# Kernel optimization log

Measured on AMD Instinct MI355X. Metric: run time of the kernel, lower is better.

The kernel has to match this reference:

```python
import jax, jax.numpy as jnp
import numpy as np

B, S, D, H = 4, 2048, 512, 8
DH = D // H


def setup_inputs() -> dict:
    key = jax.random.key(0)
    ks = jax.random.split(key, 6)
    embeddings = jax.random.normal(ks[0], (B, S, D), dtype=jnp.float32)
    token_masks = jax.random.randint(ks[1], (B, S), 0, 2, dtype=jnp.int32)
    # keras 'random_normal' initializer: stddev 0.05
    Wq = 0.05 * jax.random.normal(ks[2], (D, D), dtype=jnp.float32)
    Wk = 0.05 * jax.random.normal(ks[3], (D, D), dtype=jnp.float32)
    Wv = 0.05 * jax.random.normal(ks[4], (D, D), dtype=jnp.float32)
    Wo = 0.05 * jax.random.normal(ks[5], (D, D), dtype=jnp.float32)
    return {"embeddings": embeddings, "token_masks": token_masks,
            "Wq": Wq, "Wk": Wk, "Wv": Wv, "Wo": Wo}


def reference(embeddings, token_masks, Wq, Wk, Wv, Wo):
    b, s, d = embeddings.shape
    h, dh = H, d // H
    # QKV projections -> (b, h, s, dh)
    def split_heads(x):
        return x.reshape(b, s, h, dh).transpose(0, 2, 1, 3)
    Q = split_heads(embeddings @ Wq)
    K = split_heads(embeddings @ Wk)
    V = split_heads(embeddings @ Wv)
    scores = jnp.einsum('bhqd,bhkd->bhqk', Q, K) / jnp.sqrt(jnp.float32(dh))
    # causal (lower-triangular) mask combined with padding mask on both q and k
    causal = jnp.tril(jnp.ones((s, s), dtype=jnp.float32))
    tm = token_masks.astype(jnp.float32)
    attn_mask = causal[None, None, :, :] * tm[:, None, None, :] * tm[:, None, :, None]
    scores = jnp.where(attn_mask > 0, scores, jnp.float32(-1e30))
    weights = jax.nn.softmax(scores, axis=-1)  # dropout omitted (inference/eval mode)
    context = jnp.einsum('bhqk,bhkd->bhqd', weights, V)
    context = context.transpose(0, 2, 1, 3).reshape(b, s, d)
    return context @ Wo
```

## Files before the change

kernel.cpp:

```cpp
#include <hip/hip_runtime.h>
#include <hip/hip_bf16.h>
#include <stdint.h>

#define BATCH 4
#define SEQ 2048
#define DMODEL 512
#define NHEAD 8
#define HD 64

#define C1 0.18033688f
#define BIAS2 -23.0831207f

using f32x4 = __attribute__((ext_vector_type(4))) float;
using bfrag = __attribute__((ext_vector_type(8))) short;

__device__ __forceinline__ short f2bf(float f) {
  uint32_t x = __builtin_bit_cast(uint32_t, f);
  uint32_t r = (x + 0x7fffu + ((x >> 16) & 1u)) >> 16;
  return (short)r;
}
__device__ __forceinline__ short f2bf_fast(float f) {
  return (short)((__builtin_bit_cast(uint32_t, f) + 0x8000u) >> 16);
}
__device__ __forceinline__ float bf2f(short s) {
  return __builtin_bit_cast(float, ((uint32_t)(uint16_t)s) << 16);
}
__device__ __forceinline__ void gl_lds16(const void* g, void* l) {
  __builtin_amdgcn_global_load_lds(
      (const __attribute__((address_space(1))) void*)g,
      (__attribute__((address_space(3))) void*)l, 16, 0, 0);
}
__device__ __forceinline__ bool sniff_f32(const void* p, int tid) {
  const uint32_t* xw = (const uint32_t*)p;
  const int lane = tid & 63;
  const uint32_t w1 = xw[lane], w2 = xw[64 + lane];
  bool bad = (((w1 >> 7) & 0xffu) >= 0xB0u) | (((w1 >> 23) & 0xffu) >= 0xB0u) |
             (((w2 >> 7) & 0xffu) >= 0xB0u) | (((w2 >> 23) & 0xffu) >= 0xB0u);
  return __ballot(bad) != 0ull;
}

__global__ __launch_bounds__(256) void prep(const void* __restrict__ X,
                                            const void* __restrict__ w0,
                                            const void* __restrict__ w1,
                                            const void* __restrict__ w2,
                                            const void* __restrict__ w3,
                                            short* __restrict__ Xb,
                                            short* __restrict__ wtAll,
                                            float* __restrict__ mv) {
  const int blk = blockIdx.x, tid = threadIdx.x;
  if (blk < 2048) {
    const bool isf32 = sniff_f32(X, tid);
    const int i = (blk * 256 + tid) * 8;
    if (isf32) {
      const float* f = (const float*)X;
      short r[8];
#pragma unroll
      for (int j = 0; j < 8; ++j) r[j] = f2bf(f[i + j]);
      *(bfrag*)&Xb[i] = *(bfrag*)r;
    } else {
      *(bfrag*)&Xb[i] = *(const bfrag*)&((const short*)X)[i];
    }
  } else if (blk < 3072) {
    __shared__ short t[32][33];
    const int idx = blk - 2048;
    const int z = idx >> 8, rem = idx & 255;
    const void* in = (z == 0) ? w0 : (z == 1) ? w1 : (z == 2) ? w2 : w3;
    short* out = wtAll + (size_t)z * DMODEL * DMODEL;
    const int tx = tid & 31, ty = tid >> 5;
    const bool isf32 = sniff_f32(in, tid);
    const int n0 = (rem & 15) * 32, k0 = (rem >> 4) * 32;
#pragma unroll
    for (int i = ty; i < 32; i += 8) {
      const int idx2 = (k0 + i) * DMODEL + n0 + tx;
      t[i][tx] = isf32 ? f2bf(((const float*)in)[idx2]) : ((const short*)in)[idx2];
    }
    __syncthreads();
#pragma unroll
    for (int i = ty; i < 32; i += 8) out[(n0 + i) * DMODEL + k0 + tx] = t[tx][i];
  } else {
#pragma unroll
    for (int j = 0; j < 8; ++j) mv[tid * 8 + j] = 0.f;
  }
}

__global__ __launch_bounds__(256) void gemm_qkv(const short* __restrict__ X,
                                                const short* __restrict__ WtAll,
                                                short* __restrict__ Qo,
                                                short* __restrict__ Ko,
                                                short* __restrict__ Vo,
                                                float* __restrict__ mv) {
  __shared__ __align__(16) short As[128 * 32];
  __shared__ __align__(16) short Bs[128 * 32];
  const int which = blockIdx.z;
  const short* Wt = WtAll + which * DMODEL * DMODEL;
  const int m0 = blockIdx.y * 128, n0 = blockIdx.x * 128;
  const int tid = threadIdx.x, lane = tid & 63, wave = tid >> 6;
  const int l15 = lane & 15, quad = lane >> 4;
  const int wm = wave >> 1, wn = wave & 1;
  const int lrow = lane >> 2, lcol = (lane & 3) * 8;
  f32x4 acc[4][4] = {};
  for (int kc = 0; kc < DMODEL; kc += 32) {
#pragma unroll
    for (int i = 0; i < 2; ++i) {
      const int r0 = (wave * 2 + i) * 16;
      gl_lds16(&X[(size_t)(m0 + r0 + lrow) * DMODEL + kc + lcol], &As[r0 * 32]);
      gl_lds16(&Wt[(size_t)(n0 + r0 + lrow) * DMODEL + kc + lcol], &Bs[r0 * 32]);
    }
    __syncthreads();
    bfrag a[4], b[4];
#pragma unroll
    for (int t = 0; t < 4; ++t) {
      a[t] = *(const bfrag*)&As[(wm * 64 + t * 16 + l15) * 32 + quad * 8];
      b[t] = *(const bfrag*)&Bs[(wn * 64 + t * 16 + l15) * 32 + quad * 8];
    }
#pragma unroll
    for (int tm = 0; tm < 4; ++tm)
#pragma unroll
      for (int tn = 0; tn < 4; ++tn)
        acc[tm][tn] = __builtin_amdgcn_mfma_f32_16x16x32_bf16(a[tm], b[tn], acc[tm][tn], 0, 0, 0);
    __syncthreads();
  }
  short* O = (which == 0) ? Qo : (which == 1) ? Ko : Vo;
#pragma unroll
  for (int tn = 0; tn < 4; ++tn) {
    const int col = n0 + wn * 64 + tn * 16 + l15;
    const int h = col >> 6, d = col & 63;
#pragma unroll
    for (int tm = 0; tm < 4; ++tm) {
#pragma unroll
      for (int r = 0; r < 4; ++r) {
        const int row = m0 + wm * 64 + tm * 16 + quad * 4 + r;
        const int b = row >> 11, s = row & 2047;
        O[((b * NHEAD + h) * SEQ + s) * HD + d] = f2bf(acc[tm][tn][r]);
      }
    }
  }
  if (which == 2) {
    const int b = (m0 + wm * 64) >> 11;
#pragma unroll
    for (int tn = 0; tn < 4; ++tn) {
      float s = 0.f;
#pragma unroll
      for (int tm = 0; tm < 4; ++tm)
#pragma unroll
        for (int r = 0; r < 4; ++r) s += acc[tm][tn][r];
      s += __shfl_xor(s, 16);
      s += __shfl_xor(s, 32);
      if (quad == 0) {
        const int col = n0 + wn * 64 + tn * 16 + l15;
        const int h = col >> 6, d = col & 63;
        atomicAdd(&mv[(b * NHEAD + h) * 64 + d], s);
      }
    }
  }
}

__global__ __launch_bounds__(256) void gemm_out(const short* __restrict__ X,
                                                const short* __restrict__ Wt,
                                                float* __restrict__ O) {
  __shared__ __align__(16) short As[128 * 32];
  __shared__ __align__(16) short Bs[128 * 32];
  const int m0 = blockIdx.y * 128, n0 = blockIdx.x * 128;
  const int tid = threadIdx.x, lane = tid & 63, wave = tid >> 6;
  const int l15 = lane & 15, quad = lane >> 4;
  const int wm = wave >> 1, wn = wave & 1;
  const int lrow = lane >> 2, lcol = (lane & 3) * 8;
  f32x4 acc[4][4] = {};
  for (int kc = 0; kc < DMODEL; kc += 32) {
#pragma unroll
    for (int i = 0; i < 2; ++i) {
      const int r0 = (wave * 2 + i) * 16;
      gl_lds16(&X[(size_t)(m0 + r0 + lrow) * DMODEL + kc + lcol], &As[r0 * 32]);
      gl_lds16(&Wt[(size_t)(n0 + r0 + lrow) * DMODEL + kc + lcol], &Bs[r0 * 32]);
    }
    __syncthreads();
    bfrag a[4], b[4];
#pragma unroll
    for (int t = 0; t < 4; ++t) {
      a[t] = *(const bfrag*)&As[(wm * 64 + t * 16 + l15) * 32 + quad * 8];
      b[t] = *(const bfrag*)&Bs[(wn * 64 + t * 16 + l15) * 32 + quad * 8];
    }
#pragma unroll
    for (int tm = 0; tm < 4; ++tm)
#pragma unroll
      for (int tn = 0; tn < 4; ++tn)
        acc[tm][tn] = __builtin_amdgcn_mfma_f32_16x16x32_bf16(a[tm], b[tn], acc[tm][tn], 0, 0, 0);
    __syncthreads();
  }
#pragma unroll
  for (int tm = 0; tm < 4; ++tm)
#pragma unroll
    for (int tn = 0; tn < 4; ++tn) {
      const int col = n0 + wn * 64 + tn * 16 + l15;
#pragma unroll
      for (int r = 0; r < 4; ++r) {
        const int row = m0 + wm * 64 + tm * 16 + quad * 4 + r;
        O[(size_t)row * DMODEL + col] = acc[tm][tn][r];
      }
    }
}

__global__ __launch_bounds__(256, 4) void attn(const short* __restrict__ Q,
                                               const short* __restrict__ K,
                                               const short* __restrict__ V,
                                               const int* __restrict__ tmask,
                                               const float* __restrict__ meanV,
                                               short* __restrict__ ctx) {
  __shared__ __align__(16) short Ks[64 * 72];
  __shared__ __align__(16) short Vts[64 * 64];
  __shared__ __align__(16) short Ps[4 * 16 * 64];
  __shared__ int tmq[64];
  __shared__ int tmk[64];
  const int m2 = blockIdx.x >> 3, a3 = blockIdx.x & 7;
  const int j2 = blockIdx.y >> 3, b3 = blockIdx.y & 7;
  const int quart = (m2 + j2) & 3;
  const int qi = quart * 8 + ((quart & 1) ? (7 - a3) : a3);
  const int bh = j2 * 8 + b3;
  const int b = bh >> 3, h = bh & 7;
  const int q0 = qi * 64;
  const int tid = threadIdx.x, lane = tid & 63, wave = tid >> 6;
  const int l15 = lane & 15, quad = lane >> 4;
  const size_t base = (size_t)bh * SEQ * HD;

  bfrag qa0 = *(const bfrag*)&Q[base + (size_t)(q0 + wave * 16 + l15) * HD + quad * 8];
  bfrag qa1 = *(const bfrag*)&Q[base + (size_t)(q0 + wave * 16 + l15) * HD + 32 + quad * 8];
  if (tid < 64) tmq[tid] = tmask[b * SEQ + q0 + tid];

  f32x4 accO[4] = {};
  float lrow[4] = {0.f, 0.f, 0.f, 0.f};

  const int rp = tid >> 3, sgp = tid & 7;
  bfrag kA, kB, vA, vB;
  int tmreg = 0;

  auto prefetch = [&](int kc) {
    const size_t o0 = base + (size_t)(kc + 2 * rp) * HD + sgp * 8;
    kA = *(const bfrag*)&K[o0];
    kB = *(const bfrag*)&K[o0 + HD];
    vA = *(const bfrag*)&V[o0];
    vB = *(const bfrag*)&V[o0 + HD];
    if (tid < 64) tmreg = tmask[b * SEQ + kc + tid];
  };
  auto store_lds = [&]() {
    *(bfrag*)&Ks[(2 * rp) * 72 + sgp * 8] = kA;
    *(bfrag*)&Ks[(2 * rp + 1) * 72 + sgp * 8] = kB;
    const int g = ((rp >> 2) ^ ((sgp & 1) << 2) ^ (sgp >> 1)) & 7;
    const int kpos = (2 * rp) & 7;
#pragma unroll
    for (int j = 0; j < 8; ++j) {
      const uint32_t w = (uint32_t)(uint16_t)vA[j] | ((uint32_t)(uint16_t)vB[j] << 16);
      *(uint32_t*)&Vts[(sgp * 8 + j) * 64 + g * 8 + kpos] = w;
    }
    if (tid < 64) tmk[tid] = tmreg;
  };
  auto compute = [&](bool diag) {
    f32x4 sacc[4] = {};
#pragma unroll
    for (int t = 0; t < 4; ++t) {
      bfrag b0 = *(const bfrag*)&Ks[(t * 16 + l15) * 72 + quad * 8];
      sacc[t] = __builtin_amdgcn_mfma_f32_16x16x32_bf16(qa0, b0, sacc[t], 0, 0, 0);
    }
#pragma unroll
    for (int t = 0; t < 4; ++t) {
      bfrag b1 = *(const bfrag*)&Ks[(t * 16 + l15) * 72 + 32 + quad * 8];
      sacc[t] = __builtin_amdgcn_mfma_f32_16x16x32_bf16(qa1, b1, sacc[t], 0, 0, 0);
    }
    float badd[4];
#pragma unroll
    for (int t = 0; t < 4; ++t) badd[t] = tmk[t * 16 + l15] ? BIAS2 : -1e30f;
#pragma unroll
    for (int r = 0; r < 4; ++r) {
      const int m = quad * 4 + r;
#pragma unroll
      for (int t = 0; t < 4; ++t) {
        float p = exp2f(fmaf(sacc[t][r], C1, badd[t]));
        if (diag && (t * 16 + l15 > wave * 16 + m)) p = 0.f;
        lrow[r] += p;
        const int g = ((t * 2 + (l15 >> 3)) ^ (m & 7) ^ ((m >> 3) << 1)) & 7;
        Ps[wave * 1024 + m * 64 + g * 8 + (l15 & 7)] = f2bf_fast(p);
      }
    }
#pragma unroll
    for (int ks = 0; ks < 2; ++ks) {
#pragma unroll
      for (int t = 0; t < 4; ++t) {
        const int gp = ((ks * 4 + quad) ^ (l15 & 7) ^ ((l15 >> 3) << 1)) & 7;
        bfrag pa = *(const bfrag*)&Ps[wave * 1024 + l15 * 64 + gp * 8];
        const int d = t * 16 + l15;
        const int gv = ((ks * 4 + quad) ^ ((l15 >> 3) << 2) ^ t) & 7;
        bfrag vb = *(const bfrag*)&Vts[d * 64 + gv * 8];
        accO[t] = __builtin_amdgcn_mfma_f32_16x16x32_bf16(pa, vb, accO[t], 0, 0, 0);
      }
    }
  };

  prefetch(0);
  for (int kc = 0; kc <= q0; kc += 64) {
    __syncthreads();
    store_lds();
    __syncthreads();
    if (kc < q0) prefetch(kc + 64);
    compute(kc == q0);
  }

#pragma unroll
  for (int r = 0; r < 4; ++r) {
    float l = lrow[r];
    l += __shfl_xor(l, 1);
    l += __shfl_xor(l, 2);
    l += __shfl_xor(l, 4);
    l += __shfl_xor(l, 8);
    lrow[r] = 1.f / l;
  }
  const int qrow_loc = wave * 16 + quad * 4;
#pragma unroll
  for (int t = 0; t < 4; ++t) {
    const int d = t * 16 + l15;
    const float mvd = meanV[bh * 64 + d] * (1.f / 2048.f);
#pragma unroll
    for (int r = 0; r < 4; ++r) {
      const int row = qrow_loc + r;
      float val = accO[t][r] * lrow[r];
      if (tmq[row] == 0) val = mvd;
      ctx[((size_t)(b * SEQ + q0 + row)) * DMODEL + h * HD + d] = f2bf(val);
    }
  }
}

extern "C" void kernel_launch(void* const* d_in, const int* in_sizes, int n_in,
                              void* d_out, int out_size, void* d_ws, size_t ws_size,
                              hipStream_t stream) {
  const void* X = d_in[0];
  const int* tmask = (const int*)d_in[1];
  const void* Wq = d_in[2];
  const void* Wk = d_in[3];
  const void* Wv = d_in[4];
  const void* Wo = d_in[5];
  float* out = (float*)d_out;
  char* ws = (char*)d_ws;

  const size_t WELEM = (size_t)DMODEL * DMODEL;
  const size_t TELEM = (size_t)BATCH * NHEAD * SEQ * HD;

  float* mv = (float*)(ws + 4096);
  short* wt = (short*)(ws + 4096 + 8192);
  short* Xb = (short*)(ws + 4096 + 8192 + 2097152);
  short* Qb = Xb + TELEM;
  short* Kb = Qb + TELEM;
  short* Vb = Kb + TELEM;
  short* Cb = Vb + TELEM;

  prep<<<3073, 256, 0, stream>>>(X, Wq, Wk, Wv, Wo, Xb, wt, mv);
  gemm_qkv<<<dim3(4, 64, 3), 256, 0, stream>>>(Xb, wt, Qb, Kb, Vb, mv);
  attn<<<dim3(32, 32), 256, 0, stream>>>(Qb, Kb, Vb, tmask, mv, Cb);
  gemm_out<<<dim3(4, 64), 256, 0, stream>>>(Cb, wt + 3 * WELEM, out);
}
```

Baseline: 172.8 us.

## Split key tile across waves in attention, keep probabilities in registers

```diff
diff --git a/kernel.cpp b/kernel.cpp
--- a/kernel.cpp
+++ b/kernel.cpp
@@ -13,6 +13,8 @@
 
 using f32x4 = __attribute__((ext_vector_type(4))) float;
 using bfrag = __attribute__((ext_vector_type(8))) short;
+using u32x4 = __attribute__((ext_vector_type(4))) unsigned int;
+using s4 = __attribute__((ext_vector_type(4))) short;
 
 __device__ __forceinline__ short f2bf(float f) {
   uint32_t x = __builtin_bit_cast(uint32_t, f);
@@ -29,6 +31,11 @@
   __builtin_amdgcn_global_load_lds(
       (const __attribute__((address_space(1))) void*)g,
       (__attribute__((address_space(3))) void*)l, 16, 0, 0);
+}
+__device__ __forceinline__ uint32_t cvtpk(float lo, float hi) {
+  uint32_t r;
+  asm("v_cvt_pk_bf16_f32 %0, %1, %2" : "=v"(r) : "v"(lo), "v"(hi));
+  return r;
 }
 __device__ __forceinline__ bool sniff_f32(const void* p, int tid) {
   const uint32_t* xw = (const uint32_t*)p;
@@ -200,17 +207,15 @@
     }
 }
 
-__global__ __launch_bounds__(256, 4) void attn(const short* __restrict__ Q,
+__global__ __launch_bounds__(256, 3) void attn(const short* __restrict__ Q,
                                                const short* __restrict__ K,
                                                const short* __restrict__ V,
                                                const int* __restrict__ tmask,
                                                const float* __restrict__ meanV,
                                                short* __restrict__ ctx) {
-  __shared__ __align__(16) short Ks[64 * 72];
-  __shared__ __align__(16) short Vts[64 * 64];
-  __shared__ __align__(16) short Ps[4 * 16 * 64];
-  __shared__ int tmq[64];
-  __shared__ int tmk[64];
+  __shared__ __align__(16) short Vts[64 * 66];
+  __shared__ __align__(16) float red[4][16 * 68];
+  __shared__ float l_red[4][64];
   const int m2 = blockIdx.x >> 3, a3 = blockIdx.x & 7;
   const int j2 = blockIdx.y >> 3, b3 = blockIdx.y & 7;
   const int quart = (m2 + j2) & 3;
@@ -220,110 +225,124 @@
   const int q0 = qi * 64;
   const int tid = threadIdx.x, lane = tid & 63, wave = tid >> 6;
   const int l15 = lane & 15, quad = lane >> 4;
+  const int rp = tid >> 3, sgp = tid & 7;
   const size_t base = (size_t)bh * SEQ * HD;
 
-  bfrag qa0 = *(const bfrag*)&Q[base + (size_t)(q0 + wave * 16 + l15) * HD + quad * 8];
-  bfrag qa1 = *(const bfrag*)&Q[base + (size_t)(q0 + wave * 16 + l15) * HD + 32 + quad * 8];
-  if (tid < 64) tmq[tid] = tmask[b * SEQ + q0 + tid];
-
-  f32x4 accO[4] = {};
-  float lrow[4] = {0.f, 0.f, 0.f, 0.f};
-
-  const int rp = tid >> 3, sgp = tid & 7;
-  bfrag kA, kB, vA, vB;
-  int tmreg = 0;
+  bfrag qb[4][2];
+#pragma unroll
+  for (int qg = 0; qg < 4; ++qg) {
+    const size_t qo = base + (size_t)(q0 + qg * 16 + l15) * HD + quad * 8;
+    qb[qg][0] = *(const bfrag*)&Q[qo];
+    qb[qg][1] = *(const bfrag*)&Q[qo + 32];
+  }
+
+  f32x4 accO[4][4] = {};
+  float lq[4] = {0.f, 0.f, 0.f, 0.f};
+
+  bfrag kf0, kf1, vA, vB;
+  uint64_t km_next = 0;
 
   auto prefetch = [&](int kc) {
+    const size_t ko = base + (size_t)(kc + wave * 16 + l15) * HD + quad * 8;
+    kf0 = *(const bfrag*)&K[ko];
+    kf1 = *(const bfrag*)&K[ko + 32];
     const size_t o0 = base + (size_t)(kc + 2 * rp) * HD + sgp * 8;
-    kA = *(const bfrag*)&K[o0];
-    kB = *(const bfrag*)&K[o0 + HD];
     vA = *(const bfrag*)&V[o0];
     vB = *(const bfrag*)&V[o0 + HD];
-    if (tid < 64) tmreg = tmask[b * SEQ + kc + tid];
+    km_next = __ballot(tmask[b * SEQ + kc + lane] != 0);
   };
-  auto store_lds = [&]() {
-    *(bfrag*)&Ks[(2 * rp) * 72 + sgp * 8] = kA;
-    *(bfrag*)&Ks[(2 * rp + 1) * 72 + sgp * 8] = kB;
-    const int g = ((rp >> 2) ^ ((sgp & 1) << 2) ^ (sgp >> 1)) & 7;
-    const int kpos = (2 * rp) & 7;
+  auto store_v = [&]() {
 #pragma unroll
     for (int j = 0; j < 8; ++j) {
+      const int d = sgp * 8 + j;
       const uint32_t w = (uint32_t)(uint16_t)vA[j] | ((uint32_t)(uint16_t)vB[j] << 16);
-      *(uint32_t*)&Vts[(sgp * 8 + j) * 64 + g * 8 + kpos] = w;
-    }
-    if (tid < 64) tmk[tid] = tmreg;
-  };
-  auto compute = [&](bool diag) {
-    f32x4 sacc[4] = {};
-#pragma unroll
-    for (int t = 0; t < 4; ++t) {
-      bfrag b0 = *(const bfrag*)&Ks[(t * 16 + l15) * 72 + quad * 8];
-      sacc[t] = __builtin_amdgcn_mfma_f32_16x16x32_bf16(qa0, b0, sacc[t], 0, 0, 0);
-    }
-#pragma unroll
-    for (int t = 0; t < 4; ++t) {
-      bfrag b1 = *(const bfrag*)&Ks[(t * 16 + l15) * 72 + 32 + quad * 8];
-      sacc[t] = __builtin_amdgcn_mfma_f32_16x16x32_bf16(qa1, b1, sacc[t], 0, 0, 0);
-    }
-    float badd[4];
-#pragma unroll
-    for (int t = 0; t < 4; ++t) badd[t] = tmk[t * 16 + l15] ? BIAS2 : -1e30f;
-#pragma unroll
-    for (int r = 0; r < 4; ++r) {
-      const int m = quad * 4 + r;
-#pragma unroll
-      for (int t = 0; t < 4; ++t) {
-        float p = exp2f(fmaf(sacc[t][r], C1, badd[t]));
-        if (diag && (t * 16 + l15 > wave * 16 + m)) p = 0.f;
-        lrow[r] += p;
-        const int g = ((t * 2 + (l15 >> 3)) ^ (m & 7) ^ ((m >> 3) << 1)) & 7;
-        Ps[wave * 1024 + m * 64 + g * 8 + (l15 & 7)] = f2bf_fast(p);
-      }
-    }
-#pragma unroll
-    for (int ks = 0; ks < 2; ++ks) {
-#pragma unroll
-      for (int t = 0; t < 4; ++t) {
-        const int gp = ((ks * 4 + quad) ^ (l15 & 7) ^ ((l15 >> 3) << 1)) & 7;
-        bfrag pa = *(const bfrag*)&Ps[wave * 1024 + l15 * 64 + gp * 8];
-        const int d = t * 16 + l15;
-        const int gv = ((ks * 4 + quad) ^ ((l15 >> 3) << 2) ^ t) & 7;
-        bfrag vb = *(const bfrag*)&Vts[d * 64 + gv * 8];
-        accO[t] = __builtin_amdgcn_mfma_f32_16x16x32_bf16(pa, vb, accO[t], 0, 0, 0);
-      }
+      *(uint32_t*)&Vts[d * 66 + (rp >> 1) * 4 + (rp & 1) * 2] = w;
     }
   };
 
   prefetch(0);
   for (int kc = 0; kc <= q0; kc += 64) {
-    __syncthreads();
-    store_lds();
-    __syncthreads();
+    store_v();
+    const uint64_t km = km_next;
+    const bool diag = (kc == q0);
+    f32x4 sacc[4];
+#pragma unroll
+    for (int qg = 0; qg < 4; ++qg) {
+      f32x4 z = {};
+      z = __builtin_amdgcn_mfma_f32_16x16x32_bf16(kf0, qb[qg][0], z, 0, 0, 0);
+      sacc[qg] = __builtin_amdgcn_mfma_f32_16x16x32_bf16(kf1, qb[qg][1], z, 0, 0, 0);
+    }
     if (kc < q0) prefetch(kc + 64);
-    compute(kc == q0);
-  }
-
-#pragma unroll
-  for (int r = 0; r < 4; ++r) {
-    float l = lrow[r];
-    l += __shfl_xor(l, 1);
-    l += __shfl_xor(l, 2);
-    l += __shfl_xor(l, 4);
-    l += __shfl_xor(l, 8);
-    lrow[r] = 1.f / l;
-  }
-  const int qrow_loc = wave * 16 + quad * 4;
-#pragma unroll
-  for (int t = 0; t < 4; ++t) {
-    const int d = t * 16 + l15;
-    const float mvd = meanV[bh * 64 + d] * (1.f / 2048.f);
-#pragma unroll
-    for (int r = 0; r < 4; ++r) {
-      const int row = qrow_loc + r;
-      float val = accO[t][r] * lrow[r];
-      if (tmq[row] == 0) val = mvd;
-      ctx[((size_t)(b * SEQ + q0 + row)) * DMODEL + h * HD + d] = f2bf(val);
-    }
+    bfrag vb8[4];
+#pragma unroll
+    for (int dg = 0; dg < 4; ++dg) {
+      const int idx = (dg * 16 + l15) * 66 + (wave * 4 + quad) * 4;
+      const uint32_t lo = *(const uint32_t*)&Vts[idx];
+      const uint32_t hi = *(const uint32_t*)&Vts[idx + 2];
+      u32x4 t = {lo, hi, 0u, 0u};
+      vb8[dg] = __builtin_bit_cast(bfrag, t);
+    }
+#pragma unroll
+    for (int qg = 0; qg < 4; ++qg) {
+      float p[4];
+#pragma unroll
+      for (int r = 0; r < 4; ++r) {
+        const int kin = wave * 16 + quad * 4 + r;
+        const float badd = ((km >> kin) & 1ull) ? BIAS2 : -1e30f;
+        float pv = exp2f(fmaf(sacc[qg][r], C1, badd));
+        if (diag && (kin > qg * 16 + l15)) pv = 0.f;
+        lq[qg] += pv;
+        p[r] = pv;
+      }
+      const uint32_t w0 = cvtpk(p[0], p[1]);
+      const uint32_t w1 = cvtpk(p[2], p[3]);
+      u32x4 t = {w0, w1, 0u, 0u};
+      const bfrag pa = __builtin_bit_cast(bfrag, t);
+#pragma unroll
+      for (int dg = 0; dg < 4; ++dg)
+        accO[qg][dg] = __builtin_amdgcn_mfma_f32_16x16x32_bf16(pa, vb8[dg], accO[qg][dg], 0, 0, 0);
+    }
+  }
+
+#pragma unroll
+  for (int qg = 0; qg < 4; ++qg) {
+    lq[qg] += __shfl_xor(lq[qg], 16);
+    lq[qg] += __shfl_xor(lq[qg], 32);
+  }
+  if (quad == 0) {
+#pragma unroll
+    for (int qg = 0; qg < 4; ++qg) l_red[wave][qg * 16 + l15] = lq[qg];
+  }
+  __syncthreads();
+
+#pragma unroll
+  for (int qg = 0; qg < 4; ++qg) {
+#pragma unroll
+    for (int dg = 0; dg < 4; ++dg)
+#pragma unroll
+      for (int r = 0; r < 4; ++r)
+        red[wave][(quad * 4 + r) * 68 + dg * 16 + l15] = accO[qg][dg][r];
+    __syncthreads();
+    const int q = tid >> 4, dc = (tid & 15) * 4;
+    f32x4 s = *(const f32x4*)&red[0][q * 68 + dc];
+#pragma unroll
+    for (int w = 1; w < 4; ++w) {
+      f32x4 sw = *(const f32x4*)&red[w][q * 68 + dc];
+      s[0] += sw[0]; s[1] += sw[1]; s[2] += sw[2]; s[3] += sw[3];
+    }
+    const float lt = l_red[0][qg * 16 + q] + l_red[1][qg * 16 + q] +
+                     l_red[2][qg * 16 + q] + l_red[3][qg * 16 + q];
+    const int tq = tmask[b * SEQ + q0 + qg * 16 + q];
+    const float inv = 1.f / lt;
+    s4 o;
+#pragma unroll
+    for (int i = 0; i < 4; ++i) {
+      const float v = tq ? s[i] * inv
+                         : meanV[bh * 64 + dc + i] * (1.f / 2048.f);
+      o[i] = f2bf(v);
+    }
+    *(s4*)&ctx[((size_t)(b * SEQ + q0 + qg * 16 + q)) * DMODEL + h * HD + dc] = o;
+    if (qg != 3) __syncthreads();
   }
 }
 
```

Measured after the change: 215.8 us. +24.9%, slower.
